# Kernel tuning notes

Hardware: AMD Instinct MI355X
Metric: run time of the kernel (lower is better)

Reference implementation:

```python
import jax, jax.numpy as jnp
import numpy as np

N = 100_000          # nodes
DEG = 16             # avg degree (random edges)
E = N * DEG + N      # edges incl. self-loops (ensures no zero in-degree)
NFEAT = 256
NHID = 64
NHEADS = 8
NCLASS = 40
NEG_SLOPE = 0.2
S_F = 1.0
EPS = 1e-6


def setup_inputs() -> dict:
    key = jax.random.key(0)
    ks = jax.random.split(key, 12)
    x = jax.random.normal(ks[0], (N, NFEAT), dtype=jnp.float32)
    loops = jnp.arange(N, dtype=jnp.int32)
    src = jnp.concatenate([jax.random.randint(ks[1], (N * DEG,), 0, N, dtype=jnp.int32), loops])
    dst = jnp.concatenate([jax.random.randint(ks[2], (N * DEG,), 0, N, dtype=jnp.int32), loops])
    # layer-1: NHEADS independent single-head GATConv_G(nfeat -> nhid)
    W1 = (jax.random.normal(ks[3], (NHEADS, NHID, NFEAT), dtype=jnp.float32) * 0.05)
    al1 = jax.random.normal(ks[4], (NHEADS, NHID), dtype=jnp.float32) * 0.05
    ar1 = jax.random.normal(ks[5], (NHEADS, NHID), dtype=jnp.float32) * 0.05
    b1 = jnp.zeros((NHEADS, NHID), dtype=jnp.float32)
    p1 = jax.random.normal(ks[6], (NHEADS,), dtype=jnp.float32) * 0.1
    # layer-2: single-head GATConv_G(nhid*nheads -> nclass)
    W2 = jax.random.normal(ks[7], (NCLASS, NHID * NHEADS), dtype=jnp.float32) * 0.05
    al2 = jax.random.normal(ks[8], (NCLASS,), dtype=jnp.float32) * 0.05
    ar2 = jax.random.normal(ks[9], (NCLASS,), dtype=jnp.float32) * 0.05
    b2 = jnp.zeros((NCLASS,), dtype=jnp.float32)
    p2 = jax.random.normal(ks[10], (), dtype=jnp.float32) * 0.1
    return dict(x=x, src=src, dst=dst, W1=W1, al1=al1, ar1=ar1, b1=b1, p1=p1,
                W2=W2, al2=al2, ar2=ar2, b2=b2, p2=p2)


def _leaky_relu(x):
    return jnp.where(x >= 0, x, NEG_SLOPE * x)


def _edge_softmax(e, dst):
    # softmax over incoming edges of each destination node
    m = jax.ops.segment_max(e, dst, num_segments=N)
    ex = jnp.exp(e - m[dst])
    s = jax.ops.segment_sum(ex, dst, num_segments=N)
    return ex / s[dst]


def _gat_g_head(x, src, dst, W, al, ar, b, p):
    """One GATConv_G with num_heads=1. x:[N,Fin], W:[Fout,Fin] -> [N,Fout]."""
    ft = x @ W.T                                   # [N,Fout]
    el = ft @ al                                   # [N]
    er = ft @ ar                                   # [N]
    e = _leaky_relu(el[src] + er[dst])             # [E]
    a = _edge_softmax(e, dst)                      # [E]
    pe = jax.nn.sigmoid(p) + S_F                   # scalar, nonlinear-aggregation exponent
    mu = ft.min()                                  # global min (shift to make base positive)
    pf = jnp.power(ft - mu + EPS, pe)              # [N,Fout]
    msg = pf[src] * a[:, None]                     # [E,Fout] (u_mul_e)
    agg = jax.ops.segment_sum(msg, dst, num_segments=N)   # sum aggregation
    rst = jnp.power(agg + EPS, 1.0 / pe) + mu      # generalized-mean inverse
    return rst + b                                 # bias [Fout]


def reference(x, src, dst, W1, al1, ar1, b1, p1, W2, al2, ar2, b2, p2):
    # layer 1: NHEADS single-head GATConv_G, each with concat=True => elu, then concat
    heads = []
    for h in range(NHEADS):  # small fixed loop over structurally distinct heads
        heads.append(jax.nn.elu(_gat_g_head(x, src, dst, W1[h], al1[h], ar1[h], b1[h], p1[h])))
    hcat = jnp.concatenate(heads, axis=-1)         # [N, NHEADS*NHID]
    # layer 2: output GATConv_G (concat=False), then log_softmax classifier head
    out = _gat_g_head(hcat, src, dst, W2, al2, ar2, b2, p2)   # [N, NCLASS]
    return jax.nn.log_softmax(out, axis=-1)
```

## Files before the change

### kernel.cpp

```cpp
#include <hip/hip_runtime.h>

#define NN 100000
#define EE 1700000
#define F1 256
#define NH 8
#define HF 64
#define C1 512
#define C2 40
#define EPS 1e-6f
#define VCH 25000

#define OF_PF1   ((size_t)0)
#define OF_HCAT  (OF_PF1  + 102400000ULL)
#define OF_FT2   (OF_HCAT + 102400000ULL)
#define OF_EL1   (OF_FT2  + 16000000ULL)
#define OF_ER1   (OF_EL1  + 3200000ULL)
#define OF_EL2   (OF_ER1  + 3200000ULL)
#define OF_ER2   (OF_EL2  + 400000ULL)
#define OF_DEG   (OF_ER2  + 400000ULL)
#define OF_OFFS  (OF_DEG  + 400000ULL)
#define OF_CUR   (OF_OFFS + 400128ULL)
#define OF_SRCC  (OF_CUR  + 400000ULL)
#define OF_BSUM  (OF_SRCC + 6800000ULL)
#define OF_BOFF  (OF_BSUM + 2048ULL)
#define OF_PRM   (OF_BOFF + 2048ULL)
#define OF_W2H   (OF_PRM  + 1024ULL)
#define OF_XH    (OF_HCAT)
#define OF_WH    (OF_HCAT + 51200000ULL)
#define OF_PF2H  (OF_HCAT)


typedef _Float16 f16x8 __attribute__((ext_vector_type(8)));
typedef _Float16 f16x4 __attribute__((ext_vector_type(4)));
typedef float f32x4 __attribute__((ext_vector_type(4)));

__device__ __forceinline__ unsigned f2key(float f){
  unsigned u = __float_as_uint(f);
  return (u & 0x80000000u) ? ~u : (u | 0x80000000u);
}
__device__ __forceinline__ float key2f(unsigned k){
  unsigned u = (k & 0x80000000u) ? (k & 0x7FFFFFFFu) : ~k;
  return __uint_as_float(u);
}
__device__ __forceinline__ unsigned short f2b(float f){
  unsigned u = __float_as_uint(f);
  unsigned r = u + 0x7FFFu + ((u >> 16) & 1u);
  return (unsigned short)(r >> 16);
}
__device__ __forceinline__ float b2f(unsigned short b){
  return __uint_as_float(((unsigned)b) << 16);
}
__device__ __forceinline__ float leaky(float e){ return e >= 0.f ? e : 0.2f*e; }

__device__ __forceinline__ void gload16(const _Float16* g, char* l){
  __builtin_amdgcn_global_load_lds((const __attribute__((address_space(1))) void*)g,
                                   (__attribute__((address_space(3))) void*)l, 16, 0, 0);
}

__global__ void k_init(const float* __restrict__ p1, const float* __restrict__ p2, unsigned* __restrict__ prm){
  int t = threadIdx.x;
  float* prf = (float*)prm;
  if (t < 8){
    prm[t] = 0xFFFFFFFFu;
    float pe = 1.f/(1.f + __expf(-p1[t])) + 1.0f;
    prf[16 + t] = pe;
    prf[24 + t] = 1.f/pe;
  }
  if (t == 0){
    prm[8] = 0xFFFFFFFFu;
    float pe = 1.f/(1.f + __expf(-p2[0])) + 1.0f;
    prf[32] = pe;
    prf[33] = 1.f/pe;
  }
}

__global__ void k_zero_deg(int* __restrict__ deg){
  int i = blockIdx.x*256 + threadIdx.x;
  if (i < NN) deg[i] = 0;
}

__global__ void k_cvt16(const float* __restrict__ in, _Float16* __restrict__ out){
  int i = blockIdx.x*256 + threadIdx.x;
  const float4* p = (const float4*)in + (size_t)i*2;
  float4 a = p[0], b = p[1];
  f16x8 h = {(_Float16)a.x,(_Float16)a.y,(_Float16)a.z,(_Float16)a.w,
             (_Float16)b.x,(_Float16)b.y,(_Float16)b.z,(_Float16)b.w};
  *((f16x8*)out + i) = h;
}

__global__ void k_cvtW2(const float* __restrict__ W2, _Float16* __restrict__ W2h){
  int i = blockIdx.x*256 + threadIdx.x;
  int row = i >> 9, col = i & 511;
  W2h[i] = (row < C2) ? (_Float16)W2[row*C1 + col] : (_Float16)0.f;
}

#define G1_BM 128
#define G1_BN 128
#define G1_BK 64
__global__ __launch_bounds__(256) void k_gemm1(const _Float16* __restrict__ xh, const _Float16* __restrict__ Wh,
                                               const float* __restrict__ al1, const float* __restrict__ ar1,
                                               unsigned short* __restrict__ ft1b,
                                               float* __restrict__ el1, float* __restrict__ er1,
                                               unsigned* __restrict__ prm){
  __shared__ __align__(16) char smem[35840];
  char* Abase = smem;
  char* Bbase = smem + 16384;
  unsigned short (*Cs)[136] = (unsigned short (*)[136])smem;

  int t = threadIdx.x;
  int lane = t & 63, w = t >> 6;
  int wr = w >> 1, wc = w & 1;
  int ct = blockIdx.x * G1_BN;
  int rt = blockIdx.y * G1_BM;

  int lr8 = lane >> 3;
  int gcs = (lane & 7) ^ lr8;

  f32x4 zero = {0.f,0.f,0.f,0.f};
  f32x4 acc[4][4];
  #pragma unroll
  for (int m=0;m<4;m++)
    #pragma unroll
    for (int n=0;n<4;n++) acc[m][n] = zero;

  for (int kt = 0; kt < F1; kt += G1_BK){
    #pragma unroll
    for (int i = 0; i < 4; i++){
      int ch = w*4 + i;
      int row = ch*8 + lr8;
      int ga = min(rt + row, NN-1);
      gload16(xh + (size_t)ga*F1 + kt + gcs*8, Abase + ch*1024);
      gload16(Wh + (size_t)(ct+row)*F1 + kt + gcs*8, Bbase + ch*1024);
    }
    __syncthreads();
    #pragma unroll
    for (int kk = 0; kk < 2; kk++){
      f16x8 af[4], bf[4];
      #pragma unroll
      for (int m=0;m<4;m++){
        int row = wr*64 + m*16 + (lane & 15);
        int g = kk*4 + (lane >> 4);
        af[m] = *(f16x8*)(Abase + ((row*8 + (g ^ (row & 7)))<<4));
      }
      #pragma unroll
      for (int n=0;n<4;n++){
        int row = wc*64 + n*16 + (lane & 15);
        int g = kk*4 + (lane >> 4);
        bf[n] = *(f16x8*)(Bbase + ((row*8 + (g ^ (row & 7)))<<4));
      }
      #pragma unroll
      for (int m=0;m<4;m++)
        #pragma unroll
        for (int n=0;n<4;n++)
          acc[m][n] = __builtin_amdgcn_mfma_f32_16x16x32_f16(af[m], bf[n], acc[m][n], 0, 0, 0);
    }
    __syncthreads();
  }

  int h = (ct >> 6) + wc;
  int c0 = lane & 15;
  float alc[4], arc[4];
  #pragma unroll
  for (int n=0;n<4;n++){
    alc[n] = al1[h*HF + n*16 + c0];
    arc[n] = ar1[h*HF + n*16 + c0];
  }
  unsigned kmin = 0xFFFFFFFFu;
  #pragma unroll
  for (int m=0;m<4;m++){
    float elp[4] = {0.f,0.f,0.f,0.f};
    float erp[4] = {0.f,0.f,0.f,0.f};
    #pragma unroll
    for (int n=0;n<4;n++){
      int cl = wc*64 + n*16 + c0;
      int rl = wr*64 + m*16 + (lane >> 4)*4;
      #pragma unroll
      for (int j=0;j<4;j++){
        unsigned short ub = f2b(acc[m][n][j]);
        float vr = b2f(ub);
        Cs[rl + j][cl] = ub;
        kmin = min(kmin, f2key(vr));
        elp[j] += vr*alc[n];
        erp[j] += vr*arc[n];
      }
    }
    #pragma unroll
    for (int j=0;j<4;j++){
      #pragma unroll
      for (int off=1; off<16; off<<=1){
        elp[j] += __shfl_xor(elp[j], off);
        erp[j] += __shfl_xor(erp[j], off);
      }
      int row = rt + wr*64 + m*16 + (lane >> 4)*4 + j;
      if (c0 == 0 && row < NN){
        el1[(size_t)row*8 + h] = elp[j];
        er1[(size_t)row*8 + h] = erp[j];
      }
    }
  }
  #pragma unroll
  for (int off=1; off<64; off<<=1) kmin = min(kmin, (unsigned)__shfl_xor((int)kmin, off));
  if (lane == 0) atomicMin(&prm[h], kmin);
  __syncthreads();

  #pragma unroll
  for (int p = 0; p < 8; p++){
    int flat = p*256 + t;
    int row = flat >> 4;
    int q   = flat & 15;
    int gr = rt + row;
    if (gr < NN){
      uint4 v = *(const uint4*)&Cs[row][q*8];
      *(uint4*)&ft1b[(size_t)gr*C1 + ct + q*8] = v;
    }
  }
}

__global__ void k_count(const int* __restrict__ dst, int* __restrict__ deg){
  int e = blockIdx.x*256 + threadIdx.x;
  if (e < EE) atomicAdd(&deg[dst[e]], 1);
}
__global__ void k_scan1(const int* __restrict__ deg, int* __restrict__ offs, int* __restrict__ bsum){
  __shared__ int s[256];
  int t = threadIdx.x; int i = blockIdx.x*256 + t;
  int v = (i < NN) ? deg[i] : 0;
  s[t] = v; __syncthreads();
  for (int off=1; off<256; off<<=1){
    int tmp = (t>=off) ? s[t-off] : 0;
    __syncthreads(); s[t] += tmp; __syncthreads();
  }
  if (i < NN) offs[i] = s[t] - v;
  if (t == 255) bsum[blockIdx.x] = s[255];
}
__global__ void k_scan2(int* __restrict__ bsum, int* __restrict__ boff, int nb){
  __shared__ int s[512];
  int t = threadIdx.x;
  int v = (t < nb) ? bsum[t] : 0;
  s[t] = v; __syncthreads();
  for (int off=1; off<512; off<<=1){
    int tmp = (t>=off) ? s[t-off] : 0;
    __syncthreads(); s[t] += tmp; __syncthreads();
  }
  if (t < nb) boff[t] = s[t] - v;
}
__global__ void k_scan3(int* __restrict__ offs, int* __restrict__ cur, const int* __restrict__ boff){
  int i = blockIdx.x*256 + threadIdx.x;
  if (i < NN){
    int v = offs[i] + boff[blockIdx.x];
    offs[i] = v; cur[i] = v;
  }
  if (i == 0) offs[NN] = EE;
}
__global__ void k_fill(const int* __restrict__ src, const int* __restrict__ dst,
                       int* __restrict__ cur, int* __restrict__ srcc){
  int e = blockIdx.x*256 + threadIdx.x;
  if (e < EE){
    int d = dst[e];
    int pos = atomicAdd(&cur[d], 1);
    srcc[pos] = src[e];
  }
}

__global__ void k_pf1(unsigned short* __restrict__ ft1b, const unsigned* __restrict__ prm){
  int i = blockIdx.x*256 + threadIdx.x;
  const float* prf = (const float*)prm;
  int h = (i >> 3) & 7;
  float mu = key2f(prm[h]);
  float pe = prf[16 + h];
  uint4 q = ((const uint4*)ft1b)[i];
  unsigned r0, r1, r2, r3;
  float v0, v1;
  v0 = b2f((unsigned short)(q.x & 0xFFFFu)) - mu + EPS;
  v1 = b2f((unsigned short)(q.x >> 16)) - mu + EPS;
  r0 = (unsigned)f2b(__expf(pe*__logf(v0))) | ((unsigned)f2b(__expf(pe*__logf(v1))) << 16);
  v0 = b2f((unsigned short)(q.y & 0xFFFFu)) - mu + EPS;
  v1 = b2f((unsigned short)(q.y >> 16)) - mu + EPS;
  r1 = (unsigned)f2b(__expf(pe*__logf(v0))) | ((unsigned)f2b(__expf(pe*__logf(v1))) << 16);
  v0 = b2f((unsigned short)(q.z & 0xFFFFu)) - mu + EPS;
  v1 = b2f((unsigned short)(q.z >> 16)) - mu + EPS;
  r2 = (unsigned)f2b(__expf(pe*__logf(v0))) | ((unsigned)f2b(__expf(pe*__logf(v1))) << 16);
  v0 = b2f((unsigned short)(q.w & 0xFFFFu)) - mu + EPS;
  v1 = b2f((unsigned short)(q.w >> 16)) - mu + EPS;
  r3 = (unsigned)f2b(__expf(pe*__logf(v0))) | ((unsigned)f2b(__expf(pe*__logf(v1))) << 16);
  ((uint4*)ft1b)[i] = make_uint4(r0, r1, r2, r3);
}

__global__ __launch_bounds__(256) void k_agg1(const unsigned short* __restrict__ pf1b,
    const float* __restrict__ el1, const float* __restrict__ er1,
    const int* __restrict__ offs, const int* __restrict__ srcc,
    const float* __restrict__ b1, const unsigned* __restrict__ prm,
    _Float16* __restrict__ hcath, int vbase){
  int lane = threadIdx.x & 63; int w = threadIdx.x >> 6;
  int v = vbase + blockIdx.x*4 + w;
  if (v >= vbase + VCH) return;
  const float* prf = (const float*)prm;
  int h = lane >> 3;
  int s = lane & 7;
  int start = offs[v], end = offs[v+1];
  float erh = er1[(size_t)v*8 + h];

  float m = -INFINITY;
  for (int pos = start + s; pos < end; pos += 8){
    int u = srcc[pos];
    float e = leaky(el1[(size_t)u*8 + h] + erh);
    m = fmaxf(m, e);
  }
  m = fmaxf(m, __shfl_xor(m,1)); m = fmaxf(m, __shfl_xor(m,2)); m = fmaxf(m, __shfl_xor(m,4));
  float S = 0.f;
  for (int pos = start + s; pos < end; pos += 8){
    int u = srcc[pos];
    float e = leaky(el1[(size_t)u*8 + h] + erh);
    S += __expf(e - m);
  }
  S += __shfl_xor(S,1); S += __shfl_xor(S,2); S += __shfl_xor(S,4);
  float invS = 1.f / S;

  int es = lane >> 5;
  int hc = (lane >> 2) & 7;
  int q4 = lane & 3;
  float mh    = __shfl(m,    hc*8);
  float invSh = __shfl(invS, hc*8);
  float erhc  = __shfl(erh,  hc*8);

  float acc[16];
  #pragma unroll
  for (int j=0;j<16;j++) acc[j]=0.f;
  for (int pos = start + es; pos < end; pos += 2){
    int u = srcc[pos];
    float e = leaky(el1[(size_t)u*8 + hc] + erhc);
    float a = __expf(e - mh) * invSh;
    const unsigned short* pr = &pf1b[(size_t)u*C1 + hc*HF + q4*16];
    uint4 qa = *(const uint4*)pr;
    uint4 qb = *(const uint4*)(pr + 8);
    acc[0]  += a*b2f((unsigned short)(qa.x & 0xFFFFu));
    acc[1]  += a*b2f((unsigned short)(qa.x >> 16));
    acc[2]  += a*b2f((unsigned short)(qa.y & 0xFFFFu));
    acc[3]  += a*b2f((unsigned short)(qa.y >> 16));
    acc[4]  += a*b2f((unsigned short)(qa.z & 0xFFFFu));
    acc[5]  += a*b2f((unsigned short)(qa.z >> 16));
    acc[6]  += a*b2f((unsigned short)(qa.w & 0xFFFFu));
    acc[7]  += a*b2f((unsigned short)(qa.w >> 16));
    acc[8]  += a*b2f((unsigned short)(qb.x & 0xFFFFu));
    acc[9]  += a*b2f((unsigned short)(qb.x >> 16));
    acc[10] += a*b2f((unsigned short)(qb.y & 0xFFFFu));
    acc[11] += a*b2f((unsigned short)(qb.y >> 16));
    acc[12] += a*b2f((unsigned short)(qb.z & 0xFFFFu));
    acc[13] += a*b2f((unsigned short)(qb.z >> 16));
    acc[14] += a*b2f((unsigned short)(qb.w & 0xFFFFu));
    acc[15] += a*b2f((unsigned short)(qb.w >> 16));
  }
  #pragma unroll
  for (int j=0;j<16;j++) acc[j] += __shfl_xor(acc[j], 32);

  float mu = key2f(prm[hc]);
  float ipe = prf[24+hc];
  int fb = q4*16 + es*8;
  f16x8 o;
  #pragma unroll
  for (int j=0;j<8;j++){
    float r = __expf(ipe * __logf(acc[es*8 + j] + EPS)) + mu + b1[hc*HF + fb + j];
    o[j] = (_Float16)((r > 0.f) ? r : (__expf(r) - 1.f));
  }
  *(f16x8*)&hcath[(size_t)v*C1 + hc*HF + fb] = o;
}

__global__ __launch_bounds__(256) void k_gemm2(const _Float16* __restrict__ hcath, const _Float16* __restrict__ W2h,
    float* __restrict__ ft2, float* __restrict__ el2, float* __restrict__ er2,
    const float* __restrict__ al2, const float* __restrict__ ar2, unsigned* __restrict__ prm){
  __shared__ __align__(16) char smem[45056];
  char* Abase = smem;
  char* Bbase = smem + 32768;
  __shared__ unsigned mk;
  int t = threadIdx.x;
  int lane = t & 63, w = t >> 6;
  int rt = blockIdx.x * 128;
  if (t == 0) mk = 0xFFFFFFFFu;

  f32x4 zero = {0.f,0.f,0.f,0.f};
  f32x4 acc[2][3];
  #pragma unroll
  for (int m=0;m<2;m++)
    #pragma unroll
    for (int n=0;n<3;n++) acc[m][n] = zero;

  for (int step = 0; step < 4; step++){
    #pragma unroll
    for (int p = 0; p < 8; p++){
      int idx = p*256 + t;
      int row = idx >> 4, g = idx & 15;
      int ga = min(rt + row, NN-1);
      gload16(hcath + (size_t)ga*C1 + step*128 + ((g ^ (row & 7))<<3), Abase + idx*16);
    }
    #pragma unroll
    for (int p = 0; p < 3; p++){
      int idx = p*256 + t;
      int row = idx >> 4, g = idx & 15;
      gload16(W2h + (size_t)row*C1 + step*128 + ((g ^ (row & 7))<<3), Bbase + idx*16);
    }
    __syncthreads();
    #pragma unroll
    for (int kk = 0; kk < 4; kk++){
      f16x8 af[2], bf[3];
      #pragma unroll
      for (int m=0;m<2;m++){
        int row = w*32 + m*16 + (lane & 15);
        int g = kk*4 + (lane >> 4);
        af[m] = *(f16x8*)(Abase + ((row*16 + (g ^ (row & 7)))<<4));
      }
      #pragma unroll
      for (int n=0;n<3;n++){
        int row = n*16 + (lane & 15);
        int g = kk*4 + (lane >> 4);
        bf[n] = *(f16x8*)(Bbase + ((row*16 + (g ^ (row & 7)))<<4));
      }
      #pragma unroll
      for (int m=0;m<2;m++)
        #pragma unroll
        for (int n=0;n<3;n++)
          acc[m][n] = __builtin_amdgcn_mfma_f32_16x16x32_f16(af[m], bf[n], acc[m][n], 0, 0, 0);
    }
    __syncthreads();
  }

  int c0 = lane & 15;
  unsigned kmin = 0xFFFFFFFFu;
  #pragma unroll
  for (int m=0;m<2;m++){
    float elp[4] = {0.f,0.f,0.f,0.f};
    float erp[4] = {0.f,0.f,0.f,0.f};
    #pragma unroll
    for (int n=0;n<3;n++){
      int col = n*16 + c0;
      bool okc = (col < C2);
      float alc = okc ? al2[col] : 0.f;
      float arc = okc ? ar2[col] : 0.f;
      int rbase = rt + w*32 + m*16 + (lane >> 4)*4;
      #pragma unroll
      for (int j=0;j<4;j++){
        float vv = acc[m][n][j];
        int row = rbase + j;
        if (okc && row < NN){
          ft2[(size_t)row*C2 + col] = vv;
          elp[j] += vv*alc; erp[j] += vv*arc;
          kmin = min(kmin, f2key(vv));
        }
      }
    }
    #pragma unroll
    for (int j=0;j<4;j++){
      #pragma unroll
      for (int off=1; off<16; off<<=1){
        elp[j] += __shfl_xor(elp[j], off);
        erp[j] += __shfl_xor(erp[j], off);
      }
      int row = rt + w*32 + m*16 + (lane >> 4)*4 + j;
      if (c0 == 0 && row < NN){ el2[row] = elp[j]; er2[row] = erp[j]; }
    }
  }
  #pragma unroll
  for (int off=1; off<64; off<<=1) kmin = min(kmin, (unsigned)__shfl_xor((int)kmin, off));
  if (lane == 0) atomicMin(&mk, kmin);
  __syncthreads();
  if (t == 0) atomicMin(&prm[8], mk);
}

__global__ void k_transform2(const float* __restrict__ ft2, _Float16* __restrict__ pf2h,
                             const unsigned* __restrict__ prm){
  int i = blockIdx.x*256 + threadIdx.x;
  if (i >= NN*C2) return;
  const float* prf = (const float*)prm;
  float mu = key2f(prm[8]);
  float pe = prf[32];
  float v = ft2[i];
  pf2h[i] = (_Float16)__expf(pe * __logf(v - mu + EPS));
}

__global__ __launch_bounds__(256) void k_agg2(const _Float16* __restrict__ pf2h,
    const float* __restrict__ el2, const float* __restrict__ er2,
    const int* __restrict__ offs, const int* __restrict__ srcc,
    const float* __restrict__ b2, const unsigned* __restrict__ prm,
    float* __restrict__ out){
  int lane = threadIdx.x & 63; int w = threadIdx.x >> 6;
  int v = blockIdx.x*4 + w;
  if (v >= NN) return;
  const float* prf = (const float*)prm;
  int start = offs[v], end = offs[v+1];
  float erv = er2[v];

  float m = -INFINITY, S = 0.f;
  for (int pos = start + lane; pos < end; pos += 64){
    float e = leaky(el2[srcc[pos]] + erv);
    float d = e - m;
    if (d > 0.f){ S = S*__expf(-d) + 1.f; m = e; }
    else S += __expf(d);
  }
  float mAll = m;
  #pragma unroll
  for (int off=1; off<64; off<<=1) mAll = fmaxf(mAll, __shfl_xor(mAll, off));
  S *= __expf(m - mAll);
  #pragma unroll
  for (int off=1; off<64; off<<=1) S += __shfl_xor(S, off);
  float invS = 1.f / S;
  m = mAll;

  int s = lane >> 4;
  int c = lane & 15;
  float a0=0.f, a1=0.f, a2=0.f, a3=0.f;
  for (int pos = start + s; pos < end; pos += 4){
    int u = srcc[pos];
    float a = __expf(leaky(el2[u] + erv) - m) * invS;
    if (c < 10){
      f16x4 q = *(const f16x4*)&pf2h[(size_t)u*C2 + c*4];
      a0 += a*(float)q[0]; a1 += a*(float)q[1]; a2 += a*(float)q[2]; a3 += a*(float)q[3];
    }
  }
  a0 += __shfl_xor(a0,16); a1 += __shfl_xor(a1,16); a2 += __shfl_xor(a2,16); a3 += __shfl_xor(a3,16);
  a0 += __shfl_xor(a0,32); a1 += __shfl_xor(a1,32); a2 += __shfl_xor(a2,32); a3 += __shfl_xor(a3,32);

  float y[4];
  float mx;
  if (c < 10){
    float mu = key2f(prm[8]);
    float ipe = prf[33];
    float av[4] = {a0,a1,a2,a3};
    #pragma unroll
    for (int j=0;j<4;j++) y[j] = __expf(ipe * __logf(av[j] + EPS)) + mu + b2[c*4 + j];
    mx = fmaxf(fmaxf(y[0],y[1]), fmaxf(y[2],y[3]));
  } else {
    y[0]=y[1]=y[2]=y[3]=-INFINITY;
    mx = -INFINITY;
  }
  mx = fmaxf(mx, __shfl_xor(mx,1)); mx = fmaxf(mx, __shfl_xor(mx,2));
  mx = fmaxf(mx, __shfl_xor(mx,4)); mx = fmaxf(mx, __shfl_xor(mx,8));
  float se = 0.f;
  if (c < 10){
    #pragma unroll
    for (int j=0;j<4;j++) se += __expf(y[j] - mx);
  }
  se += __shfl_xor(se,1); se += __shfl_xor(se,2); se += __shfl_xor(se,4); se += __shfl_xor(se,8);
  float ls = __logf(se);
  if (s == 0 && c < 10){
    float4 o = make_float4(y[0]-mx-ls, y[1]-mx-ls, y[2]-mx-ls, y[3]-mx-ls);
    *(float4*)&out[(size_t)v*C2 + c*4] = o;
  }
}

extern "C" void kernel_launch(void* const* d_in, const int* in_sizes, int n_in,
                              void* d_out, int out_size, void* d_ws, size_t ws_size,
                              hipStream_t stream){
  const float* x   = (const float*)d_in[0];
  const int*   src = (const int*)d_in[1];
  const int*   dst = (const int*)d_in[2];
  const float* W1  = (const float*)d_in[3];
  const float* al1 = (const float*)d_in[4];
  const float* ar1 = (const float*)d_in[5];
  const float* b1  = (const float*)d_in[6];
  const float* p1  = (const float*)d_in[7];
  const float* W2  = (const float*)d_in[8];
  const float* al2 = (const float*)d_in[9];
  const float* ar2 = (const float*)d_in[10];
  const float* b2  = (const float*)d_in[11];
  const float* p2  = (const float*)d_in[12];
  float* out = (float*)d_out;
  char* ws = (char*)d_ws;

  unsigned short* pf1b  = (unsigned short*)(ws + OF_PF1);
  _Float16* hcath = (_Float16*)(ws + OF_HCAT);
  _Float16* xh  = (_Float16*)(ws + OF_XH);
  _Float16* Wh  = (_Float16*)(ws + OF_WH);
  _Float16* W2h = (_Float16*)(ws + OF_W2H);
  _Float16* pf2h = (_Float16*)(ws + OF_PF2H);
  float* ft2   = (float*)(ws + OF_FT2);
  float* el1   = (float*)(ws + OF_EL1);
  float* er1   = (float*)(ws + OF_ER1);
  float* el2   = (float*)(ws + OF_EL2);
  float* er2   = (float*)(ws + OF_ER2);
  int*   deg   = (int*)(ws + OF_DEG);
  int*   offs  = (int*)(ws + OF_OFFS);
  int*   cur   = (int*)(ws + OF_CUR);
  int*   srcc  = (int*)(ws + OF_SRCC);
  int*   bsum  = (int*)(ws + OF_BSUM);
  int*   boff  = (int*)(ws + OF_BOFF);
  unsigned* prm = (unsigned*)(ws + OF_PRM);

  const int NB1 = (NN + 255)/256;
  const int NBE = (EE + 255)/256;

  k_init<<<1, 64, 0, stream>>>(p1, p2, prm);
  k_zero_deg<<<NB1, 256, 0, stream>>>(deg);
  k_cvt16<<<12500, 256, 0, stream>>>(x, xh);
  k_cvt16<<<64, 256, 0, stream>>>(W1, Wh);
  k_cvtW2<<<96, 256, 0, stream>>>(W2, W2h);
  k_gemm1<<<dim3(C1/G1_BN, (NN + G1_BM - 1)/G1_BM), 256, 0, stream>>>(xh, Wh, al1, ar1, pf1b, el1, er1, prm);
  k_count<<<NBE, 256, 0, stream>>>(dst, deg);
  k_scan1<<<NB1, 256, 0, stream>>>(deg, offs, bsum);
  k_scan2<<<1, 512, 0, stream>>>(bsum, boff, NB1);
  k_scan3<<<NB1, 256, 0, stream>>>(offs, cur, boff);
  k_fill<<<NBE, 256, 0, stream>>>(src, dst, cur, srcc);
  k_pf1<<<25000, 256, 0, stream>>>(pf1b, prm);
  k_agg1<<<VCH/4, 256, 0, stream>>>(pf1b, el1, er1, offs, srcc, b1, prm, hcath, 0);
  k_agg1<<<VCH/4, 256, 0, stream>>>(pf1b, el1, er1, offs, srcc, b1, prm, hcath, 25000);
  k_agg1<<<VCH/4, 256, 0, stream>>>(pf1b, el1, er1, offs, srcc, b1, prm, hcath, 50000);
  k_agg1<<<VCH/4, 256, 0, stream>>>(pf1b, el1, er1, offs, srcc, b1, prm, hcath, 75000);
  k_gemm2<<<(NN + 127)/128, 256, 0, stream>>>(hcath, W2h, ft2, el2, er2, al2, ar2, prm);
  k_transform2<<<(NN*C2 + 255)/256, 256, 0, stream>>>(ft2, pf2h, prm);
  k_agg2<<<NN/4, 256, 0, stream>>>(pf2h, el2, er2, offs, srcc, b2, prm, out);
}
```

Measured before the change: 901.3 us.

## Load full-K A tile once in gemm1, read W from global; merge agg1 launches

The first GEMM now stages the whole 128x256 fp16 A tile in 64KB of LDS up front with a swizzled layout, and then runs all eight K-groups without the per-K-step barriers. B fragments are read directly from global memory (the small, cache-resident W) instead of going through LDS. Separately, the four chunked layer-1 aggregation launches are collapsed into one launch over all nodes. The 64KB LDS footprint lowers occupancy and removes the overlap between loading and MFMA, in exchange for fewer syncs and less LDS traffic.

```diff
diff --git a/kernel.cpp b/kernel.cpp
--- a/kernel.cpp
+++ b/kernel.cpp
@@ -8,7 +8,6 @@
 #define C1 512
 #define C2 40
 #define EPS 1e-6f
-#define VCH 25000
 
 #define OF_PF1   ((size_t)0)
 #define OF_HCAT  (OF_PF1  + 102400000ULL)
@@ -96,15 +95,13 @@
 
 #define G1_BM 128
 #define G1_BN 128
-#define G1_BK 64
 __global__ __launch_bounds__(256) void k_gemm1(const _Float16* __restrict__ xh, const _Float16* __restrict__ Wh,
                                                const float* __restrict__ al1, const float* __restrict__ ar1,
                                                unsigned short* __restrict__ ft1b,
                                                float* __restrict__ el1, float* __restrict__ er1,
                                                unsigned* __restrict__ prm){
-  __shared__ __align__(16) char smem[35840];
+  __shared__ __align__(16) char smem[65536];
   char* Abase = smem;
-  char* Bbase = smem + 16384;
   unsigned short (*Cs)[136] = (unsigned short (*)[136])smem;
 
   int t = threadIdx.x;
@@ -113,8 +110,15 @@
   int ct = blockIdx.x * G1_BN;
   int rt = blockIdx.y * G1_BM;
 
-  int lr8 = lane >> 3;
-  int gcs = (lane & 7) ^ lr8;
+  #pragma unroll
+  for (int p = 0; p < 16; p++){
+    int idx = p*256 + t;
+    int row = idx >> 5, gs = idx & 31;
+    int glog = ((gs & 7) ^ (row & 7)) | (gs & 24);
+    int ga = min(rt + row, NN-1);
+    gload16(xh + (size_t)ga*F1 + glog*8, Abase + idx*16);
+  }
+  __syncthreads();
 
   f32x4 zero = {0.f,0.f,0.f,0.f};
   f32x4 acc[4][4];
@@ -123,39 +127,31 @@
     #pragma unroll
     for (int n=0;n<4;n++) acc[m][n] = zero;
 
-  for (int kt = 0; kt < F1; kt += G1_BK){
-    #pragma unroll
-    for (int i = 0; i < 4; i++){
-      int ch = w*4 + i;
-      int row = ch*8 + lr8;
-      int ga = min(rt + row, NN-1);
-      gload16(xh + (size_t)ga*F1 + kt + gcs*8, Abase + ch*1024);
-      gload16(Wh + (size_t)(ct+row)*F1 + kt + gcs*8, Bbase + ch*1024);
-    }
-    __syncthreads();
-    #pragma unroll
-    for (int kk = 0; kk < 2; kk++){
-      f16x8 af[4], bf[4];
-      #pragma unroll
-      for (int m=0;m<4;m++){
-        int row = wr*64 + m*16 + (lane & 15);
-        int g = kk*4 + (lane >> 4);
-        af[m] = *(f16x8*)(Abase + ((row*8 + (g ^ (row & 7)))<<4));
-      }
-      #pragma unroll
-      for (int n=0;n<4;n++){
-        int row = wc*64 + n*16 + (lane & 15);
-        int g = kk*4 + (lane >> 4);
-        bf[n] = *(f16x8*)(Bbase + ((row*8 + (g ^ (row & 7)))<<4));
-      }
-      #pragma unroll
-      for (int m=0;m<4;m++)
-        #pragma unroll
-        for (int n=0;n<4;n++)
-          acc[m][n] = __builtin_amdgcn_mfma_f32_16x16x32_f16(af[m], bf[n], acc[m][n], 0, 0, 0);
-    }
-    __syncthreads();
-  }
+  int arow0 = wr*64 + (lane & 15);
+  int brow0 = ct + wc*64 + (lane & 15);
+  int ksub  = (lane >> 4)*8;
+
+  #pragma unroll
+  for (int kg = 0; kg < 8; kg++){
+    int g = kg*4 + (lane >> 4);
+    f16x8 af[4], bf[4];
+    #pragma unroll
+    for (int m=0;m<4;m++){
+      int row = arow0 + m*16;
+      int gslot = ((g & 7) ^ (row & 7)) | (g & 24);
+      af[m] = *(f16x8*)(Abase + ((row*32 + gslot)<<4));
+    }
+    #pragma unroll
+    for (int n=0;n<4;n++){
+      bf[n] = *(const f16x8*)(Wh + (size_t)(brow0 + n*16)*F1 + kg*32 + ksub);
+    }
+    #pragma unroll
+    for (int m=0;m<4;m++)
+      #pragma unroll
+      for (int n=0;n<4;n++)
+        acc[m][n] = __builtin_amdgcn_mfma_f32_16x16x32_f16(af[m], bf[n], acc[m][n], 0, 0, 0);
+  }
+  __syncthreads();
 
   int h = (ct >> 6) + wc;
   int c0 = lane & 15;
@@ -289,10 +285,10 @@
     const float* __restrict__ el1, const float* __restrict__ er1,
     const int* __restrict__ offs, const int* __restrict__ srcc,
     const float* __restrict__ b1, const unsigned* __restrict__ prm,
-    _Float16* __restrict__ hcath, int vbase){
+    _Float16* __restrict__ hcath){
   int lane = threadIdx.x & 63; int w = threadIdx.x >> 6;
-  int v = vbase + blockIdx.x*4 + w;
-  if (v >= vbase + VCH) return;
+  int v = blockIdx.x*4 + w;
+  if (v >= NN) return;
   const float* prf = (const float*)prm;
   int h = lane >> 3;
   int s = lane & 7;
@@ -598,10 +594,7 @@
   k_scan3<<<NB1, 256, 0, stream>>>(offs, cur, boff);
   k_fill<<<NBE, 256, 0, stream>>>(src, dst, cur, srcc);
   k_pf1<<<25000, 256, 0, stream>>>(pf1b, prm);
-  k_agg1<<<VCH/4, 256, 0, stream>>>(pf1b, el1, er1, offs, srcc, b1, prm, hcath, 0);
-  k_agg1<<<VCH/4, 256, 0, stream>>>(pf1b, el1, er1, offs, srcc, b1, prm, hcath, 25000);
-  k_agg1<<<VCH/4, 256, 0, stream>>>(pf1b, el1, er1, offs, srcc, b1, prm, hcath, 50000);
-  k_agg1<<<VCH/4, 256, 0, stream>>>(pf1b, el1, er1, offs, srcc, b1, prm, hcath, 75000);
+  k_agg1<<<NN/4, 256, 0, stream>>>(pf1b, el1, er1, offs, srcc, b1, prm, hcath);
   k_gemm2<<<(NN + 127)/128, 256, 0, stream>>>(hcath, W2h, ft2, el2, er2, al2, ar2, prm);
   k_transform2<<<(NN*C2 + 255)/256, 256, 0, stream>>>(ft2, pf2h, prm);
   k_agg2<<<NN/4, 256, 0, stream>>>(pf2h, el2, er2, offs, srcc, b2, prm, out);
```

After: 881.7 us. -2.2%, faster.
